# Performance work log

Measured on AMD Instinct MI355X. Metric: run time of the kernel, lower is better.

## Reference

```python
import jax, jax.numpy as jnp
import numpy as np

SH_C0 = 0.28209479177387814
SH_C1 = 0.4886025119029199
SH_C2 = (1.0925484305920792, -1.0925484305920792, 0.31539156525252005, -1.0925484305920792, 0.5462742152960396)
SH_C3 = (-0.5900435899266435, 2.890611442640554, -0.4570457994644658, 0.3731763325901154, -0.4570457994644658, 1.445305721320277, -0.5900435899266435)

BG = 128  # gaussians per compositing block


def quat_to_rot(q):
    # q: [N,4] normalized quaternion (w,x,y,z) -> [N,3,3]
    w, x, y, z = q[:, 0], q[:, 1], q[:, 2], q[:, 3]
    R = jnp.stack([
        1 - 2 * (y * y + z * z), 2 * (x * y - w * z), 2 * (x * z + w * y),
        2 * (x * y + w * z), 1 - 2 * (x * x + z * z), 2 * (y * z - w * x),
        2 * (x * z - w * y), 2 * (y * z + w * x), 1 - 2 * (x * x + y * y)],
        axis=-1)
    return R.reshape(-1, 3, 3)


def eval_sh(sh, d):
    # sh: [N,16,3] degree-3 SH coeffs; d: [N,3] unit view dirs -> [N,3] rgb
    x, y, z = d[:, 0:1], d[:, 1:2], d[:, 2:3]
    xx, yy, zz = x * x, y * y, z * z
    xy, yz, xz = x * y, y * z, x * z
    res = SH_C0 * sh[:, 0]
    res = res - SH_C1 * y * sh[:, 1] + SH_C1 * z * sh[:, 2] - SH_C1 * x * sh[:, 3]
    res = (res + SH_C2[0] * xy * sh[:, 4] + SH_C2[1] * yz * sh[:, 5]
           + SH_C2[2] * (2 * zz - xx - yy) * sh[:, 6]
           + SH_C2[3] * xz * sh[:, 7] + SH_C2[4] * (xx - yy) * sh[:, 8])
    res = (res + SH_C3[0] * y * (3 * xx - yy) * sh[:, 9] + SH_C3[1] * xy * z * sh[:, 10]
           + SH_C3[2] * y * (4 * zz - xx - yy) * sh[:, 11]
           + SH_C3[3] * z * (2 * zz - 3 * xx - 3 * yy) * sh[:, 12]
           + SH_C3[4] * x * (4 * zz - xx - yy) * sh[:, 13]
           + SH_C3[5] * z * (xx - yy) * sh[:, 14] + SH_C3[6] * x * (xx - 3 * yy) * sh[:, 15])
    return res


def gs_forward(pws, shs, alphas_raw, scales_raw, rots_raw, us, Rcw, tcw, intr, height, width):
    fx, fy, cx, cy = intr[0], intr[1], intr[2], intr[3]
    N = pws.shape[0]
    HW = height * width

    # activations (GSModel.forward)
    alphas = jax.nn.sigmoid(alphas_raw[:, 0])          # [N]
    scales = jnp.exp(scales_raw)                       # [N,3]
    rots = rots_raw / jnp.linalg.norm(rots_raw, axis=1, keepdims=True)

    # gsc.project
    pcs = pws @ Rcw.T + tcw                            # [N,3] camera frame
    depth = pcs[:, 2]
    zs = jnp.where(depth > 0.2, depth, 1.0)            # safe divide for culled pts
    u = jnp.stack([fx * pcs[:, 0] / zs + cx, fy * pcs[:, 1] / zs + cy], axis=-1)
    # the `us` input is a grad-capture dummy; forward value comes from projection
    u = u + us - jax.lax.stop_gradient(us)

    # gsc.computeCov3D: Cov3d = (R S)(R S)^T
    R = quat_to_rot(rots)
    M = R * scales[:, None, :]
    cov3d = M @ jnp.swapaxes(M, 1, 2)                  # [N,3,3]

    # gsc.computeCov2D: cov2d = J W Cov3d W^T J^T + 0.3 I
    tanfx = width / (2.0 * fx)
    tanfy = height / (2.0 * fy)
    tx = jnp.clip(pcs[:, 0] / zs, -1.3 * tanfx, 1.3 * tanfx) * zs
    ty = jnp.clip(pcs[:, 1] / zs, -1.3 * tanfy, 1.3 * tanfy) * zs
    zero = jnp.zeros_like(zs)
    J = jnp.stack([
        fx / zs, zero, -fx * tx / (zs * zs),
        zero, fy / zs, -fy * ty / (zs * zs)], axis=-1).reshape(N, 2, 3)
    T = jnp.einsum('nij,jk->nik', J, Rcw)              # [N,2,3]
    cov2d = jnp.einsum('nij,njk,nlk->nil', T, cov3d, T)
    cov2d = cov2d + 0.3 * jnp.eye(2, dtype=cov2d.dtype)
    a, b, c = cov2d[:, 0, 0], cov2d[:, 0, 1], cov2d[:, 1, 1]
    det = a * c - b * b
    valid = (depth > 0.2) & (det > 0)
    det_s = jnp.where(valid, det, 1.0)

    # gsc.inverseCov2D: conic + screen-space radius (areas)
    cinv = jnp.stack([c / det_s, -b / det_s, a / det_s], axis=-1)  # [N,3]
    mid = 0.5 * (a + c)
    lam = mid + jnp.sqrt(jnp.maximum(mid * mid - det, 0.1))
    radius = jnp.where(valid, jnp.ceil(3.0 * jnp.sqrt(lam)), 0.0)
    areas = jnp.stack([radius, radius], axis=-1)       # [N,2]

    # gsc.sh2Color
    twc = -Rcw.T @ tcw
    dirs = pws - twc
    dirs = dirs / jnp.linalg.norm(dirs, axis=1, keepdims=True)
    colors = jnp.maximum(eval_sh(shs.reshape(N, 16, 3), dirs) + 0.5, 0.0)  # [N,3]

    # gsc.splat: depth-sorted front-to-back alpha compositing over all pixels
    order = jnp.argsort(depth)
    nb = N // BG
    u_s = u[order].reshape(nb, BG, 2)
    cinv_s = cinv[order].reshape(nb, BG, 3)
    al_s = alphas[order].reshape(nb, BG)
    col_s = colors[order].reshape(nb, BG, 3)
    val_s = valid[order].reshape(nb, BG)

    ys, xs = jnp.meshgrid(jnp.arange(height, dtype=jnp.float32),
                          jnp.arange(width, dtype=jnp.float32), indexing='ij')
    px = xs.ravel()
    py = ys.ravel()

    @jax.checkpoint
    def body(carry, blk):
        logT, acc = carry                              # [HW], [3,HW]
        ub, cb, ab, colb, vb = blk
        dx = px[None, :] - ub[:, 0:1]                  # [BG,HW]
        dy = py[None, :] - ub[:, 1:2]
        power = -0.5 * (cb[:, 0:1] * dx * dx + cb[:, 2:3] * dy * dy) - cb[:, 1:2] * dx * dy
        alp = jnp.minimum(0.99, ab[:, None] * jnp.exp(power))
        alp = jnp.where((power <= 0) & (alp >= 1.0 / 255.0) & vb[:, None], alp, 0.0)
        l1m = jnp.log1p(-alp)
        cs = jnp.cumsum(l1m, axis=0)
        logT_i = logT[None, :] + jnp.concatenate(
            [jnp.zeros((1, HW), l1m.dtype), cs[:-1]], axis=0)  # exclusive transmittance
        Ti = jnp.exp(logT_i)
        w = jnp.where(Ti > 1e-4, alp * Ti, 0.0)        # early-termination at tau<1e-4
        acc = acc + jnp.einsum('gp,gc->cp', w, colb)
        return (logT + cs[-1], acc), None

    init = (jnp.zeros(HW, dtype=jnp.float32), jnp.zeros((3, HW), dtype=jnp.float32))
    (_, acc), _ = jax.lax.scan(body, init, (u_s, cinv_s, al_s, col_s, val_s))
    image = acc.reshape(3, height, width)
    return image, areas


def setup_inputs() -> dict:
    key = jax.random.key(0)
    ks = jax.random.split(key, 6)
    N, H, W = 8192, 256, 256
    pws = jax.random.normal(ks[0], (N, 3), jnp.float32) * 2.0 + jnp.array([0.0, 0.0, 6.0])
    shs = jax.random.normal(ks[1], (N, 48), jnp.float32) * 0.3
    alphas_raw = jax.random.normal(ks[2], (N, 1), jnp.float32)
    scales_raw = jax.random.normal(ks[3], (N, 3), jnp.float32) * 0.3 - 3.0
    rots_raw = jax.random.normal(ks[4], (N, 4), jnp.float32)
    us = jnp.zeros((N, 2), jnp.float32)
    Rcw = jnp.eye(3, dtype=jnp.float32)
    tcw = jnp.zeros((3,), jnp.float32)
    intr = jnp.array([400.0, 400.0, 128.0, 128.0], jnp.float32)  # fx, fy, cx, cy
    return {"pws": pws, "shs": shs, "alphas_raw": alphas_raw, "scales_raw": scales_raw,
            "rots_raw": rots_raw, "us": us, "Rcw": Rcw, "tcw": tcw, "intr": intr,
            "height": H, "width": W}


def reference(pws, shs, alphas_raw, scales_raw, rots_raw, us, Rcw, tcw, intr, height, width):
    return gs_forward(pws, shs, alphas_raw, scales_raw, rots_raw, us, Rcw, tcw, intr, height, width)
```

## Files before the change

kernel.cpp:

```cpp
#include <hip/hip_runtime.h>

__global__ __launch_bounds__(256) void k_pre(
    const float* __restrict__ pws, const float* __restrict__ shs,
    const float* __restrict__ alphas_raw, const float* __restrict__ scales_raw,
    const float* __restrict__ rots_raw, const float* __restrict__ Rcw,
    const float* __restrict__ tcw, const float* __restrict__ intr,
    int N, int W, int H, float* __restrict__ areas,
    unsigned long long* __restrict__ keys, unsigned* __restrict__ rank,
    float* __restrict__ P)
{
    int i = blockIdx.x * 256 + threadIdx.x;
    if (i >= N) return;
    rank[i] = 0u;

    float R00=Rcw[0],R01=Rcw[1],R02=Rcw[2];
    float R10=Rcw[3],R11=Rcw[4],R12=Rcw[5];
    float R20=Rcw[6],R21=Rcw[7],R22=Rcw[8];
    float t0=tcw[0],t1=tcw[1],t2=tcw[2];
    float fx=intr[0],fy=intr[1],cx=intr[2],cy=intr[3];

    float pwx=pws[i*3+0], pwy=pws[i*3+1], pwz=pws[i*3+2];
    float pcx = R00*pwx + R01*pwy + R02*pwz + t0;
    float pcy = R10*pwx + R11*pwy + R12*pwz + t1;
    float pcz = R20*pwx + R21*pwy + R22*pwz + t2;
    float depth = pcz;
    float zs = (depth > 0.2f) ? depth : 1.0f;
    float u0 = fx * pcx / zs + cx;
    float u1 = fy * pcy / zs + cy;

    float qw=rots_raw[i*4+0], qx=rots_raw[i*4+1], qy=rots_raw[i*4+2], qz=rots_raw[i*4+3];
    float qn = sqrtf(qw*qw + qx*qx + qy*qy + qz*qz);
    qw/=qn; qx/=qn; qy/=qn; qz/=qn;
    float s0 = expf(scales_raw[i*3+0]);
    float s1 = expf(scales_raw[i*3+1]);
    float s2 = expf(scales_raw[i*3+2]);

    float xx=qx*qx, yy=qy*qy, zq=qz*qz;
    float xy=qx*qy, xz=qx*qz, yz=qy*qz;
    float wx=qw*qx, wy=qw*qy, wz=qw*qz;
    float r00=1.f-2.f*(yy+zq), r01=2.f*(xy-wz),     r02=2.f*(xz+wy);
    float r10=2.f*(xy+wz),     r11=1.f-2.f*(xx+zq), r12=2.f*(yz-wx);
    float r20=2.f*(xz-wy),     r21=2.f*(yz+wx),     r22=1.f-2.f*(xx+yy);

    float m00=r00*s0, m01=r01*s1, m02=r02*s2;
    float m10=r10*s0, m11=r11*s1, m12=r12*s2;
    float m20=r20*s0, m21=r21*s1, m22=r22*s2;
    float V00=m00*m00+m01*m01+m02*m02;
    float V01=m00*m10+m01*m11+m02*m12;
    float V02=m00*m20+m01*m21+m02*m22;
    float V11=m10*m10+m11*m11+m12*m12;
    float V12=m10*m20+m11*m21+m12*m22;
    float V22=m20*m20+m21*m21+m22*m22;

    float tanfx = (float)W / (2.f*fx), tanfy = (float)H / (2.f*fy);
    float limx = 1.3f*tanfx, limy = 1.3f*tanfy;
    float txl = fminf(fmaxf(pcx/zs, -limx), limx) * zs;
    float tyl = fminf(fmaxf(pcy/zs, -limy), limy) * zs;
    float iz = 1.f/zs, iz2 = iz*iz;
    float J00 = fx*iz, J02 = -fx*txl*iz2;
    float J11 = fy*iz, J12 = -fy*tyl*iz2;

    float T00=J00*R00+J02*R20, T01=J00*R01+J02*R21, T02=J00*R02+J02*R22;
    float T10=J11*R10+J12*R20, T11=J11*R11+J12*R21, T12=J11*R12+J12*R22;
    float A0=T00*V00+T01*V01+T02*V02;
    float A1=T00*V01+T01*V11+T02*V12;
    float A2=T00*V02+T01*V12+T02*V22;
    float B0=T10*V00+T11*V01+T12*V02;
    float B1=T10*V01+T11*V11+T12*V12;
    float B2=T10*V02+T11*V12+T12*V22;
    float ca = A0*T00+A1*T01+A2*T02 + 0.3f;
    float cb = A0*T10+A1*T11+A2*T12;
    float cc = B0*T10+B1*T11+B2*T12 + 0.3f;

    float det = ca*cc - cb*cb;
    bool valid = (depth > 0.2f) && (det > 0.f);
    float det_s = valid ? det : 1.f;
    float dinv = 1.f/det_s;
    float ci0 =  cc*dinv, ci1 = -cb*dinv, ci2 = ca*dinv;
    float mid = 0.5f*(ca+cc);
    float lam = mid + sqrtf(fmaxf(mid*mid - det, 0.1f));
    float radius = valid ? ceilf(3.f*sqrtf(lam)) : 0.f;
    areas[2*i+0] = radius;
    areas[2*i+1] = radius;

    float alpha = 1.f/(1.f + expf(-alphas_raw[i]));

    float tw0 = -(R00*t0 + R10*t1 + R20*t2);
    float tw1 = -(R01*t0 + R11*t1 + R21*t2);
    float tw2 = -(R02*t0 + R12*t1 + R22*t2);
    float dx_=pwx-tw0, dy_=pwy-tw1, dz_=pwz-tw2;
    float dn = sqrtf(dx_*dx_+dy_*dy_+dz_*dz_);
    float x=dx_/dn, y=dy_/dn, z=dz_/dn;
    float sxx=x*x, syy=y*y, szz=z*z;
    float sxy=x*y, syz=y*z, sxz=x*z;
    const float* sh = shs + i*48;
    float col[3];
    #pragma unroll
    for (int c = 0; c < 3; ++c) {
        float res = 0.28209479177387814f*sh[0*3+c];
        res += -0.4886025119029199f*y*sh[1*3+c]
             +  0.4886025119029199f*z*sh[2*3+c]
             + -0.4886025119029199f*x*sh[3*3+c];
        res +=  1.0925484305920792f*sxy*sh[4*3+c]
             + -1.0925484305920792f*syz*sh[5*3+c]
             +  0.31539156525252005f*(2.f*szz-sxx-syy)*sh[6*3+c]
             + -1.0925484305920792f*sxz*sh[7*3+c]
             +  0.5462742152960396f*(sxx-syy)*sh[8*3+c];
        res += -0.5900435899266435f*y*(3.f*sxx-syy)*sh[9*3+c]
             +  2.890611442640554f*sxy*z*sh[10*3+c]
             + -0.4570457994644658f*y*(4.f*szz-sxx-syy)*sh[11*3+c]
             +  0.3731763325901154f*z*(2.f*szz-3.f*sxx-3.f*syy)*sh[12*3+c]
             + -0.4570457994644658f*x*(4.f*szz-sxx-syy)*sh[13*3+c]
             +  1.445305721320277f*z*(sxx-syy)*sh[14*3+c]
             + -0.5900435899266435f*x*(sxx-3.f*syy)*sh[15*3+c];
        col[c] = fmaxf(res + 0.5f, 0.f);
    }

    float rc2;
    if (!valid || 255.f*alpha < 0.999f) {
        rc2 = -1.f;
    } else {
        float r2 = 2.f*lam*logf(255.f*alpha);
        float r  = sqrtf(fmaxf(r2, 0.f)) + 1.f;
        rc2 = r*r;
    }

    P[0*N+i]=u0;  P[1*N+i]=u1;  P[2*N+i]=ci0; P[3*N+i]=ci1; P[4*N+i]=ci2;
    P[5*N+i]=alpha; P[6*N+i]=col[0]; P[7*N+i]=col[1]; P[8*N+i]=col[2];
    P[9*N+i]=rc2;

    unsigned ud = __float_as_uint(depth);
    ud = (ud & 0x80000000u) ? ~ud : (ud | 0x80000000u);
    keys[i] = ((unsigned long long)ud << 32) | (unsigned)i;
}

#define JC 512
__global__ __launch_bounds__(256) void k_rank_scatter(
    const unsigned long long* __restrict__ keys, int N,
    unsigned* __restrict__ rank, const float* __restrict__ Pun,
    float4* __restrict__ gA, float4* __restrict__ gB,
    float4* __restrict__ cull)
{
    __shared__ unsigned long long sk[JC];
    const int j0 = blockIdx.y * JC;
    const int nJ = gridDim.y;
    for (int t = threadIdx.x; t < JC; t += 256) {
        int j = j0 + t;
        sk[t] = (j < N) ? keys[j] : ~0ull;
    }
    __syncthreads();

    const int i0 = blockIdx.x * 512 + threadIdx.x;
    const int i1 = i0 + 256;
    unsigned long long my0 = (i0 < N) ? keys[i0] : 0ull;
    unsigned long long my1 = (i1 < N) ? keys[i1] : 0ull;

    int c0 = 0, c1 = 0;
    const ulonglong2* sk2 = (const ulonglong2*)sk;
    #pragma unroll 4
    for (int t = 0; t < JC/2; ++t) {
        ulonglong2 kk = sk2[t];
        c0 += (kk.x < my0) ? 1 : 0;
        c0 += (kk.y < my0) ? 1 : 0;
        c1 += (kk.x < my1) ? 1 : 0;
        c1 += (kk.y < my1) ? 1 : 0;
    }
    if (i0 < N) {
        unsigned old = atomicAdd(&rank[i0], (unsigned)c0 + (1u << 20));
        if ((int)(old >> 20) == nJ - 1) {
            int s = (int)(old & 0xFFFFFu) + c0;
            cull[s] = make_float4(Pun[0*N+i0], Pun[1*N+i0], Pun[9*N+i0], 0.f);
            gA[s]   = make_float4(Pun[2*N+i0], Pun[3*N+i0], Pun[4*N+i0], Pun[5*N+i0]);
            gB[s]   = make_float4(Pun[6*N+i0], Pun[7*N+i0], Pun[8*N+i0], 0.f);
        }
    }
    if (i1 < N) {
        unsigned old = atomicAdd(&rank[i1], (unsigned)c1 + (1u << 20));
        if ((int)(old >> 20) == nJ - 1) {
            int s = (int)(old & 0xFFFFFu) + c1;
            cull[s] = make_float4(Pun[0*N+i1], Pun[1*N+i1], Pun[9*N+i1], 0.f);
            gA[s]   = make_float4(Pun[2*N+i1], Pun[3*N+i1], Pun[4*N+i1], Pun[5*N+i1]);
            gB[s]   = make_float4(Pun[6*N+i1], Pun[7*N+i1], Pun[8*N+i1], 0.f);
        }
    }
}

__global__ __launch_bounds__(256) void k_render(
    const float4* __restrict__ gA, const float4* __restrict__ gB,
    const float4* __restrict__ cull, int N, int W, int H,
    float* __restrict__ out)
{
    const int tid = threadIdx.x;
    const int tilesX = (W + 15) >> 4;
    const int tile = blockIdx.x;
    const int tX = tile % tilesX, tY = tile / tilesX;
    const int ix = (tX << 4) + (tid & 15);
    const int iy = (tY << 4) + (tid >> 4);
    const bool inb = (ix < W) && (iy < H);
    const float pxf = (float)ix, pyf = (float)iy;
    const float tx0 = (float)(tX << 4), ty0 = (float)(tY << 4);
    int tx1i = (tX << 4) + 15; if (tx1i > W-1) tx1i = W-1;
    int ty1i = (tY << 4) + 15; if (ty1i > H-1) ty1i = H-1;
    const float tx1 = (float)tx1i, ty1 = (float)ty1i;

    float T = inb ? 1.f : 0.f;
    float aR = 0.f, aG = 0.f, aB = 0.f;

    __shared__ float4 sG0[256];
    __shared__ float4 sG1[256];
    __shared__ float  sB2[256];
    __shared__ unsigned long long sMask[4];

    const int wave = tid >> 6, lane = tid & 63;

    for (int base = 0; base < N; base += 256) {
        int g = base + tid;
        bool ov = false;
        float u0=0.f, u1=0.f;
        float4 a4 = make_float4(0.f,0.f,0.f,0.f);
        float4 b4 = make_float4(0.f,0.f,0.f,0.f);
        if (g < N) {
            float4 cu = cull[g];
            u0 = cu.x; u1 = cu.y;
            float cxp = fminf(fmaxf(u0, tx0), tx1);
            float cyp = fminf(fmaxf(u1, ty0), ty1);
            float ddx = u0 - cxp, ddy = u1 - cyp;
            ov = (ddx*ddx + ddy*ddy) <= cu.z;
            if (ov) { a4 = gA[g]; b4 = gB[g]; }
        }
        unsigned long long m = __ballot(ov);
        if (lane == 0) sMask[wave] = m;
        __syncthreads();
        int cnt = 0, off = 0;
        #pragma unroll
        for (int w2 = 0; w2 < 4; ++w2) {
            int pc = __popcll(sMask[w2]);
            if (w2 < wave) off += pc;
            cnt += pc;
        }
        if (ov) {
            int pos = off + __popcll(m & ((1ull << lane) - 1ull));
            sG0[pos] = make_float4(u0, u1, a4.x, a4.y);
            sG1[pos] = make_float4(a4.z, a4.w, b4.x, b4.y);
            sB2[pos] = b4.z;
        }
        __syncthreads();

        for (int e = 0; e < cnt; ++e) {
            float4 e0 = sG0[e];
            float4 e1 = sG1[e];
            float  gb = sB2[e];
            float ddx = pxf - e0.x, ddy = pyf - e0.y;
            float power = -0.5f*(e0.z*ddx*ddx + e1.x*ddy*ddy) - e0.w*ddx*ddy;
            float alp = fminf(0.99f, e1.y * __expf(power));
            alp = (power <= 0.f && alp >= (1.0f/255.0f)) ? alp : 0.f;
            float w = (T > 0.0001f) ? alp * T : 0.f;
            aR = fmaf(w, e1.z, aR);
            aG = fmaf(w, e1.w, aG);
            aB = fmaf(w, gb, aB);
            T = T - T * alp;
        }
        int done = (T <= 0.0001f) ? 1 : 0;
        if (__syncthreads_and(done)) break;
    }

    if (inb) {
        int HW = W * H;
        int pix = iy * W + ix;
        out[pix]        = aR;
        out[HW + pix]   = aG;
        out[2*HW + pix] = aB;
    }
}

extern "C" void kernel_launch(void* const* d_in, const int* in_sizes, int n_in,
                              void* d_out, int out_size, void* d_ws, size_t ws_size,
                              hipStream_t stream) {
    const float* pws        = (const float*)d_in[0];
    const float* shs        = (const float*)d_in[1];
    const float* alphas_raw = (const float*)d_in[2];
    const float* scales_raw = (const float*)d_in[3];
    const float* rots_raw   = (const float*)d_in[4];
    const float* Rcw        = (const float*)d_in[6];
    const float* tcw        = (const float*)d_in[7];
    const float* intr       = (const float*)d_in[8];

    const int N  = in_sizes[0] / 3;
    const int HW = (out_size - 2 * N) / 3;
    int W = 1; while ((long long)W * W < (long long)HW) ++W;
    const int H = HW / W;

    float* out   = (float*)d_out;
    float* areas = out + 3 * HW;

    char* ws = (char*)d_ws;
    size_t off = 0;
    unsigned long long* keys = (unsigned long long*)(ws + off); off += (size_t)N * 8;
    unsigned* rank = (unsigned*)(ws + off);                     off += (size_t)N * 4;
    off = (off + 15) & ~(size_t)15;
    float* Pun = (float*)(ws + off);                            off += (size_t)10 * N * 4;
    off = (off + 15) & ~(size_t)15;
    float4* cullv = (float4*)(ws + off);                        off += (size_t)N * 16;
    float4* gA = (float4*)(ws + off);                           off += (size_t)N * 16;
    float4* gB = (float4*)(ws + off);                           off += (size_t)N * 16;

    int gsN = (N + 255) / 256;
    k_pre<<<gsN, 256, 0, stream>>>(pws, shs, alphas_raw, scales_raw, rots_raw,
                                   Rcw, tcw, intr, N, W, H, areas, keys, rank, Pun);
    dim3 rgrid((N + 511) / 512, (N + JC - 1) / JC);
    k_rank_scatter<<<rgrid, 256, 0, stream>>>(keys, N, rank, Pun, gA, gB, cullv);
    int tilesX = (W + 15) / 16, tilesY = (H + 15) / 16;
    int nTiles = tilesX * tilesY;
    k_render<<<nTiles, 256, 0, stream>>>(gA, gB, cullv, N, W, H, out);
}
```

Baseline: 129.3 us.

## Split compositing across depth segments with single-wave 8x8 tiles and combine pass

The render kernel now uses 8x8 pixel tiles, one 64-lane wave per block, so the block-wide barriers and mask exchange are replaced by a single ballot. The sorted gaussian list is cut into up to 8 depth segments composited in parallel, each writing partial transmittance and colour to a workspace buffer. A new combine kernel merges the segments front to back. This adds far more blocks and exposes more parallelism, at the cost of an extra kernel, segment-buffer traffic and less early termination, since later segments cannot stop on saturation from earlier ones.

```diff
diff --git a/kernel.cpp b/kernel.cpp
--- a/kernel.cpp
+++ b/kernel.cpp
@@ -185,67 +185,57 @@
     }
 }
 
-__global__ __launch_bounds__(256) void k_render(
+__global__ __launch_bounds__(64) void k_render(
     const float4* __restrict__ gA, const float4* __restrict__ gB,
     const float4* __restrict__ cull, int N, int W, int H,
-    float* __restrict__ out)
+    int nTiles, int nseg, float4* __restrict__ segbuf)
 {
-    const int tid = threadIdx.x;
-    const int tilesX = (W + 15) >> 4;
-    const int tile = blockIdx.x;
+    const int lane = threadIdx.x;
+    const int tilesX = (W + 7) >> 3;
+    const int tile = blockIdx.x % nTiles, seg = blockIdx.x / nTiles;
     const int tX = tile % tilesX, tY = tile / tilesX;
-    const int ix = (tX << 4) + (tid & 15);
-    const int iy = (tY << 4) + (tid >> 4);
+    const int ix = (tX << 3) + (lane & 7);
+    const int iy = (tY << 3) + (lane >> 3);
     const bool inb = (ix < W) && (iy < H);
     const float pxf = (float)ix, pyf = (float)iy;
-    const float tx0 = (float)(tX << 4), ty0 = (float)(tY << 4);
-    int tx1i = (tX << 4) + 15; if (tx1i > W-1) tx1i = W-1;
-    int ty1i = (tY << 4) + 15; if (ty1i > H-1) ty1i = H-1;
+    const float tx0 = (float)(tX << 3), ty0 = (float)(tY << 3);
+    int tx1i = (tX << 3) + 7; if (tx1i > W-1) tx1i = W-1;
+    int ty1i = (tY << 3) + 7; if (ty1i > H-1) ty1i = H-1;
     const float tx1 = (float)tx1i, ty1 = (float)ty1i;
+
+    const int per = (N + nseg - 1) / nseg;
+    const int g0 = seg * per;
+    const int g1 = min(N, g0 + per);
 
     float T = inb ? 1.f : 0.f;
     float aR = 0.f, aG = 0.f, aB = 0.f;
 
-    __shared__ float4 sG0[256];
-    __shared__ float4 sG1[256];
-    __shared__ float  sB2[256];
-    __shared__ unsigned long long sMask[4];
-
-    const int wave = tid >> 6, lane = tid & 63;
-
-    for (int base = 0; base < N; base += 256) {
-        int g = base + tid;
+    __shared__ float4 sG0[64];
+    __shared__ float4 sG1[64];
+    __shared__ float  sB2[64];
+
+    for (int base = g0; base < g1; base += 64) {
+        int g = base + lane;
         bool ov = false;
-        float u0=0.f, u1=0.f;
-        float4 a4 = make_float4(0.f,0.f,0.f,0.f);
-        float4 b4 = make_float4(0.f,0.f,0.f,0.f);
-        if (g < N) {
+        float u0 = 0.f, u1 = 0.f;
+        if (g < g1) {
             float4 cu = cull[g];
             u0 = cu.x; u1 = cu.y;
             float cxp = fminf(fmaxf(u0, tx0), tx1);
             float cyp = fminf(fmaxf(u1, ty0), ty1);
             float ddx = u0 - cxp, ddy = u1 - cyp;
             ov = (ddx*ddx + ddy*ddy) <= cu.z;
-            if (ov) { a4 = gA[g]; b4 = gB[g]; }
         }
         unsigned long long m = __ballot(ov);
-        if (lane == 0) sMask[wave] = m;
-        __syncthreads();
-        int cnt = 0, off = 0;
-        #pragma unroll
-        for (int w2 = 0; w2 < 4; ++w2) {
-            int pc = __popcll(sMask[w2]);
-            if (w2 < wave) off += pc;
-            cnt += pc;
-        }
+        int cnt = __popcll(m);
         if (ov) {
-            int pos = off + __popcll(m & ((1ull << lane) - 1ull));
+            int pos = __popcll(m & ((1ull << lane) - 1ull));
+            float4 a4 = gA[g];
+            float4 b4 = gB[g];
             sG0[pos] = make_float4(u0, u1, a4.x, a4.y);
             sG1[pos] = make_float4(a4.z, a4.w, b4.x, b4.y);
             sB2[pos] = b4.z;
         }
-        __syncthreads();
-
         for (int e = 0; e < cnt; ++e) {
             float4 e0 = sG0[e];
             float4 e1 = sG1[e];
@@ -260,17 +250,30 @@
             aB = fmaf(w, gb, aB);
             T = T - T * alp;
         }
-        int done = (T <= 0.0001f) ? 1 : 0;
-        if (__syncthreads_and(done)) break;
+        if (__all(T <= 0.0001f)) break;
     }
 
     if (inb) {
-        int HW = W * H;
         int pix = iy * W + ix;
-        out[pix]        = aR;
-        out[HW + pix]   = aG;
-        out[2*HW + pix] = aB;
-    }
+        segbuf[(size_t)seg * (size_t)(W*H) + pix] = make_float4(T, aR, aG, aB);
+    }
+}
+
+__global__ __launch_bounds__(256) void k_combine(
+    const float4* __restrict__ segbuf, int HW, int nseg,
+    float* __restrict__ out)
+{
+    int p = blockIdx.x * 256 + threadIdx.x;
+    if (p >= HW) return;
+    float T = 1.f, r = 0.f, g = 0.f, b = 0.f;
+    for (int s = 0; s < nseg; ++s) {
+        float4 v = segbuf[(size_t)s * HW + p];
+        r = fmaf(T, v.y, r);
+        g = fmaf(T, v.z, g);
+        b = fmaf(T, v.w, b);
+        T *= v.x;
+    }
+    out[p] = r; out[HW + p] = g; out[2*HW + p] = b;
 }
 
 extern "C" void kernel_launch(void* const* d_in, const int* in_sizes, int n_in,
@@ -303,13 +306,19 @@
     float4* cullv = (float4*)(ws + off);                        off += (size_t)N * 16;
     float4* gA = (float4*)(ws + off);                           off += (size_t)N * 16;
     float4* gB = (float4*)(ws + off);                           off += (size_t)N * 16;
+    float4* segbuf = (float4*)(ws + off);
+    size_t remain = (ws_size > off) ? (ws_size - off) : 0;
+    int nseg = 8;
+    while (nseg > 1 && (size_t)nseg * (size_t)HW * 16 > remain) nseg >>= 1;
 
     int gsN = (N + 255) / 256;
     k_pre<<<gsN, 256, 0, stream>>>(pws, shs, alphas_raw, scales_raw, rots_raw,
                                    Rcw, tcw, intr, N, W, H, areas, keys, rank, Pun);
     dim3 rgrid((N + 511) / 512, (N + JC - 1) / JC);
     k_rank_scatter<<<rgrid, 256, 0, stream>>>(keys, N, rank, Pun, gA, gB, cullv);
-    int tilesX = (W + 15) / 16, tilesY = (H + 15) / 16;
+    int tilesX = (W + 7) / 8, tilesY = (H + 7) / 8;
     int nTiles = tilesX * tilesY;
-    k_render<<<nTiles, 256, 0, stream>>>(gA, gB, cullv, N, W, H, out);
-}
+    k_render<<<nTiles * nseg, 64, 0, stream>>>(gA, gB, cullv, N, W, H,
+                                               nTiles, nseg, segbuf);
+    k_combine<<<(HW + 255) / 256, 256, 0, stream>>>(segbuf, HW, nseg, out);
+}
```

Result: faster. 110.3 us (-14.7%).
